# Kernel optimization log

Measured on AMD Instinct MI355X. Metric: run time of the kernel, lower is better.

## Reference

```python
import jax, jax.numpy as jnp
import numpy as np
from jax import lax

B, HCH, NCODES, H, W = 16, 32, 256, 256, 256

def conv2d(x, w, b, pad):
    y = lax.conv_general_dilated(x, w, (1, 1), [(pad, pad), (pad, pad)],
                                 dimension_numbers=('NCHW', 'OIHW', 'NCHW'))
    return y + b[None, :, None, None]

def vq(z, codebook):
    # z: (B,C,H,W); codebook: (K,C)
    zf = jnp.transpose(z, (0, 2, 3, 1)).reshape(-1, z.shape[1])  # (BHW,C)
    dists = (zf ** 2).sum(1, keepdims=True) + (codebook ** 2).sum(1) - 2.0 * zf @ codebook.T
    idx = jnp.argmin(dists, axis=1)
    zq = codebook[idx].reshape(z.shape[0], z.shape[2], z.shape[3], z.shape[1])
    zq = jnp.transpose(zq, (0, 3, 1, 2))
    # straight-through estimator
    return z + lax.stop_gradient(zq - z)

def setup_inputs() -> dict:
    key = jax.random.key(0)
    ks = jax.random.split(key, 12)
    s = lambda k, shp, scale=0.1: (jax.random.normal(k, shp, jnp.float32) * scale)
    return {
        'x': jax.random.normal(ks[0], (B, 1, H, W), jnp.float32),
        'stem_w': s(ks[1], (HCH, 1, 3, 3)),
        'stem_b': s(ks[2], (HCH,)),
        'up1_w': s(ks[3], (HCH, HCH, 3, 3)),
        'up1_b': s(ks[4], (HCH,)),
        'up2_w': s(ks[5], (HCH, HCH, 1, 1)),
        'up2_b': s(ks[6], (HCH,)),
        'tau_w': s(ks[7], (HCH, HCH, 1, 1)),
        'tau_b': s(ks[8], (HCH,)),
        'codebook': jax.random.uniform(ks[9], (NCODES, HCH), jnp.float32,
                                       -1.0 / NCODES, 1.0 / NCODES),
        'dec_w': s(ks[10], (1, HCH, 1, 1)),
        'dec_b': s(ks[11], (1,)),
        'n_steps': 5,
    }

def reference(x, stem_w, stem_b, up1_w, up1_b, up2_w, up2_b, tau_w, tau_b,
              codebook, dec_w, dec_b, n_steps):
    state = jax.nn.relu(conv2d(x, stem_w, stem_b, 1))
    for t in range(n_steps):
        delta = conv2d(jax.nn.relu(conv2d(state, up1_w, up1_b, 1)), up2_w, up2_b, 0)
        beta = jax.nn.sigmoid(conv2d(state, tau_w, tau_b, 0))
        state = beta * state + (1.0 - beta) * delta
        state = vq(state, codebook)  # vq_every = 1
    return jax.nn.sigmoid(conv2d(state, dec_w, dec_b, 0))
```

## Files before the change

kernel.cpp:

```cpp
#include <hip/hip_runtime.h>
#include <hip/hip_bf16.h>

#define BATCH 16
#define HH 256
#define WW 256
#define NPIX (BATCH*HH*WW)
#define NSTEPS 5
#define CBS 40
#define HS  258
#define HIMG (HS*HS)

#define W1P 0
#define W2P 9216
#define WTP 10240
#define IDP 11264
#define CBP 12288
#define FRAGS_TOT 20480

using u16 = unsigned short;
using u32 = unsigned int;
using u8  = unsigned char;

typedef __attribute__((ext_vector_type(8))) short bf8_t;
typedef __attribute__((ext_vector_type(4))) float f4_t;
typedef __attribute__((ext_vector_type(2))) float f2_t;

#define MFMA16 __builtin_amdgcn_mfma_f32_16x16x32_bf16

#define DPPMIN(v, CTRL) do { \
    u32 _o = (u32)__builtin_amdgcn_update_dpp((int)(v), (int)(v), (CTRL), 0xF, 0xF, false); \
    (v) = _o < (v) ? _o : (v); } while (0)

#define LDS_ORDER() asm volatile("" ::: "memory")

__device__ __forceinline__ float bf2f(u32 u) {
    union { u32 i; float f; } v; v.i = u << 16; return v.f;
}
__device__ __forceinline__ u16 f2bf(float f) {
    union { float f; u32 i; } v; v.f = f;
    u32 x = v.i;
    x += 0x7fffu + ((x >> 16) & 1u);
    return (u16)(x >> 16);
}
__device__ __forceinline__ u32 pack2bf(float a, float b) {
    __hip_bfloat162 h2 = __float22bfloat162_rn(float2{a, b});
    union { __hip_bfloat162 h; u32 u; } v; v.h = h2; return v.u;
}
__device__ __forceinline__ float ldin(const void* p, int i, int f32) {
    return f32 ? ((const float*)p)[i] : bf2f(((const u16*)p)[i]);
}
__device__ __forceinline__ u16 ldbf(const void* p, int i, int f32) {
    return f32 ? f2bf(((const float*)p)[i]) : ((const u16*)p)[i];
}
__device__ __forceinline__ int sniff_f32(const void* xraw) {
    const u32* xw = (const u32*)xraw;
    int cnt = 0;
    for (int j = 0; j < 64; j++) {
        u32 w = xw[j];
        float flo = bf2f(w & 0xffffu);
        float a = fabsf(flo);
        if (flo == 0.0f || (a >= 6e-8f && a <= 64.0f)) cnt++;
    }
    return (cnt < 32) ? 1 : 0;
}
__device__ __forceinline__ int chperm(int kp) { return (kp >> 1) | ((kp & 1) << 4); }

__global__ void prep_kernel(const void* x,
    const void* stem_w, const void* stem_b, const void* up1_w, const void* up1_b,
    const void* up2_w, const void* up2_b, const void* tau_w, const void* tau_b,
    const void* cb, const void* dec_w, const void* dec_b,
    u16* frags, u16* cb_bf, u16* idxh_a, u16* idxh_b,
    float* cn2, float* cadj, float* decdot, float* wf0,
    float* up1_bf, float* up2_bf, float* tau_bf, float* stem_bf, int* flag)
{
    int f32 = sniff_f32(x);
    int i = blockIdx.x * 256 + threadIdx.x;
    if (i == 0) *flag = f32;
    if (i < 9216) {
        int slot = i >> 9, rem = i & 511, lane = rem >> 3, j = rem & 7;
        int tap = slot >> 1, nt = slot & 1;
        int co = nt*16 + (lane & 15), ci = chperm((lane >> 4)*8 + j);
        frags[W1P + i] = ldbf(up1_w, (co*32+ci)*9 + tap, f32);
        return;
    }
    i -= 9216;
    if (i < 1024) {
        int nt = i >> 9, rem = i & 511, lane = rem >> 3, j = rem & 7;
        int co = nt*16 + (lane & 15), k = chperm((lane >> 4)*8 + j);
        frags[W2P + i] = f2bf(-0.25f * ldin(up2_w, co*32 + k, f32));
        return;
    }
    i -= 1024;
    if (i < 1024) {
        int nt = i >> 9, rem = i & 511, lane = rem >> 3, j = rem & 7;
        int co = nt*16 + (lane & 15), k = chperm((lane >> 4)*8 + j);
        frags[WTP + i] = ldbf(tau_w, co*32 + k, f32);
        return;
    }
    i -= 1024;
    if (i < 1024) {
        int s = i >> 9, rem = i & 511, lane = rem >> 3, j = rem & 7;
        int colq = lane & 15, quad = lane >> 4;
        int ch = chperm(quad*8 + j);
        frags[IDP + i] = (ch == (colq + s*16)) ? (u16)0xBE80 : (u16)0;
        return;
    }
    i -= 1024;
    if (i < 8192) {
        int nt = i >> 9, rem = i & 511, lane = rem >> 3, j = rem & 7;
        int code = nt*16 + (lane & 15), c = chperm((lane >> 4)*8 + j);
        frags[CBP + i] = ldbf(cb, code*32 + c, f32);
        return;
    }
    i -= 8192;
    if (i < 257*CBS) {
        int row = i / CBS, p = i - row*CBS;
        cb_bf[i] = (p < 32 && row < 256) ? ldbf(cb, row*32 + chperm(p), f32) : (u16)0;
        return;
    }
    i -= 257*CBS;
    if (i < 16448) {
        int bb = i / 1028, r = i - bb*1028;
        int row, colh;
        if (r < 258)      { row = 0;            colh = r; }
        else if (r < 516) { row = 257;          colh = r - 258; }
        else if (r < 774) { row = r - 516 + 1;  colh = 0; }
        else              { row = r - 774 + 1;  colh = 257; }
        int a = bb*HIMG + row*HS + colh;
        idxh_a[a] = 256; idxh_b[a] = 256;
        return;
    }
    i -= 16448;
    if (i < 256) {
        float s = 0.f;
        for (int c = 0; c < 32; c++) { float v = ldin(cb, i*32+c, f32); s += v*v; }
        cn2[i] = 0.5f * s;
        return;
    }
    i -= 256;
    if (i < 256) {
        float s = 0.f;
        for (int c = 0; c < 32; c++) { float v = ldin(cb, i*32+c, f32); s += v*v; }
        cadj[i] = 0.25f * (0.5f * s) + 0.5f;
        return;
    }
    i -= 256;
    if (i < 256) {
        float s = ldin(dec_b, 0, f32);
        for (int c = 0; c < 32; c++) s += ldin(dec_w, c, f32) * ldin(cb, i*32+c, f32);
        decdot[i] = s;
        return;
    }
    i -= 256;
    if (i < 288) {
        int tap = i >> 5, e = i & 31;
        int co = (e >> 1) + (e & 1)*16;
        wf0[i] = ldin(stem_w, co*9 + tap, f32);
        return;
    }
    i -= 288;
    if (i < 32) { up1_bf[i]  = ldin(up1_b, i, f32); return; }
    i -= 32;
    if (i < 32) { up2_bf[i]  = -0.25f * ldin(up2_b, i, f32); return; }
    i -= 32;
    if (i < 32) { tau_bf[i]  = ldin(tau_b, i, f32); return; }
    i -= 32;
    if (i < 32) {
        int co = (i >> 1) + (i & 1)*16;
        stem_bf[i] = ldin(stem_b, co, f32);
        return;
    }
}

__global__ __launch_bounds__(512) void step0_kernel(
    const void* __restrict__ xraw, const int* __restrict__ flagp,
    u16* __restrict__ idx_out,
    const u16* __restrict__ fragsg, const float* __restrict__ cn2,
    const float* __restrict__ up1_b, const float* __restrict__ up2_b,
    const float* __restrict__ tau_b, const float* __restrict__ wf0,
    const float* __restrict__ stem_bf)
{
    __shared__ __align__(16) u16 smem[34944];
    u16* w1f   = smem;
    u16* w2f   = smem + 9216;
    u16* wtf   = smem + 10240;
    u16* tileq = smem + 11264;
    u16* hzb   = smem + 30848;
    float* xs  = (float*)hzb;

    const u16* __restrict__ cbg = fragsg + CBP;

    int tid = threadIdx.x;
    int lane = tid & 63, wave = tid >> 6;
    int col = lane & 15, quad = lane >> 4;
    int b = blockIdx.z, x0 = blockIdx.x * 16, y0 = blockIdx.y * 32;

    bf8_t id0 = *(const bf8_t*)&fragsg[IDP + (0*64+lane)*8];
    bf8_t id1 = *(const bf8_t*)&fragsg[IDP + (1*64+lane)*8];

    {
        const uint4* s4 = (const uint4*)(fragsg + W1P);
        uint4* d4 = (uint4*)smem;
        for (int i = tid; i < 1408; i += 512) d4[i] = s4[i];
    }

    {
        int f32 = *flagp;
        for (int pp = tid; pp < 720; pp += 512) {
            int r = pp / 20, c = pp - r*20;
            int gy = y0 - 2 + r, gx = x0 - 2 + c;
            float v = 0.f;
            if ((unsigned)gy < 256u && (unsigned)gx < 256u)
                v = ldin(xraw, (b << 16) | (gy << 8) | gx, f32);
            xs[pp] = v;
        }
        __syncthreads();
        const f2_t* wb2 = (const f2_t*)stem_bf;
        for (int pp = tid; pp < 612; pp += 512) {
            int r = pp / 18, c = pp - r*18;
            int gy = y0 - 1 + r, gx = x0 - 1 + c;
            uint4 qv[4] = {{0,0,0,0},{0,0,0,0},{0,0,0,0},{0,0,0,0}};
            if ((unsigned)gy < 256u && (unsigned)gx < 256u) {
                f2_t acc2[16];
#pragma unroll
                for (int m = 0; m < 16; m++) acc2[m] = wb2[m];
#pragma unroll
                for (int tap = 0; tap < 9; tap++) {
                    float v = xs[(r + tap/3)*20 + (c + tap%3)];
                    f2_t vv = {v, v};
                    const f2_t* w2 = (const f2_t*)&wf0[tap*32];
#pragma unroll
                    for (int m = 0; m < 16; m++)
                        acc2[m] = __builtin_elementwise_fma(vv, w2[m], acc2[m]);
                }
                u32* ow = (u32*)qv;
#pragma unroll
                for (int m = 0; m < 16; m++)
                    ow[m] = pack2bf(fmaxf(acc2[m][0], 0.f), fmaxf(acc2[m][1], 0.f));
            }
#pragma unroll
            for (int q = 0; q < 4; q++)
                *(uint4*)&tileq[(q*612 + pp)*8] = qv[q];
        }
    }
    __syncthreads();

    float cn2adj[16];
#pragma unroll
    for (int nt = 0; nt < 16; nt++) cn2adj[nt] = 0.25f*cn2[nt*16+col] + 0.5f;
    float bu1C0 = up1_b[col], bu1C1 = up1_b[col+16];
    float bu2_0 = up2_b[col], bu2_1 = up2_b[col+16];
    float bt0 = tau_b[col],   bt1 = tau_b[col+16];
    u16* hzw = &hzb[wave*512];
    u32* hz32 = (u32*)hzw;
    int wy = wave * 4;
    f4_t kz = {0.f,0.f,0.f,0.f};

    bf8_t rows[4][3];
#pragma unroll
    for (int i = 0; i < 4; i++)
#pragma unroll
        for (int dx = 0; dx < 3; dx++)
            rows[i][dx] = *(const bf8_t*)&tileq[(quad*612 + (wy+i)*18 + col+dx)*8];

#pragma unroll
    for (int rrp = 0; rrp < 2; rrp++) {
        if (rrp) {
#pragma unroll
            for (int dx = 0; dx < 3; dx++) {
                rows[0][dx] = rows[2][dx];
                rows[1][dx] = rows[3][dx];
                rows[2][dx] = *(const bf8_t*)&tileq[(quad*612 + (wy+4)*18 + col+dx)*8];
                rows[3][dx] = *(const bf8_t*)&tileq[(quad*612 + (wy+5)*18 + col+dx)*8];
            }
        }
        f4_t aA0 = kz, aA1 = kz, aB0 = kz, aB1 = kz;
#pragma unroll
        for (int t = 0; t < 9; t++) {
            int dy = t/3, dx = t - dy*3;
            bf8_t wA = *(const bf8_t*)&w1f[((t*2+0)*64 + lane)*8];
            bf8_t wB = *(const bf8_t*)&w1f[((t*2+1)*64 + lane)*8];
            aA0 = MFMA16(rows[dy  ][dx], wA, aA0, 0, 0, 0);
            aA1 = MFMA16(rows[dy  ][dx], wB, aA1, 0, 0, 0);
            aB0 = MFMA16(rows[dy+1][dx], wA, aB0, 0, 0, 0);
            aB1 = MFMA16(rows[dy+1][dx], wB, aB1, 0, 0, 0);
        }
#pragma unroll
        for (int r = 0; r < 4; r++) {
            int px = quad*4 + r;
            hz32[px*16 + col] = pack2bf(fmaxf(aA0[r] + bu1C0, 0.f),
                                        fmaxf(aA1[r] + bu1C1, 0.f));
        }
        LDS_ORDER();
        bf8_t hA0 = *(const bf8_t*)&hzw[col*32 + quad*8];
        LDS_ORDER();
#pragma unroll
        for (int r = 0; r < 4; r++) {
            int px = quad*4 + r;
            hz32[px*16 + col] = pack2bf(fmaxf(aB0[r] + bu1C0, 0.f),
                                        fmaxf(aB1[r] + bu1C1, 0.f));
        }
        LDS_ORDER();
        bf8_t hA1 = *(const bf8_t*)&hzw[col*32 + quad*8];
        LDS_ORDER();

        bf8_t w20 = *(const bf8_t*)&w2f[(0*64+lane)*8];
        bf8_t w21 = *(const bf8_t*)&w2f[(1*64+lane)*8];
        bf8_t wt0 = *(const bf8_t*)&wtf[(0*64+lane)*8];
        bf8_t wt1 = *(const bf8_t*)&wtf[(1*64+lane)*8];
        bf8_t sA0 = rows[1][1], sA1 = rows[2][1];
        f4_t d00 = MFMA16(hA0, w20, kz, 0, 0, 0);
        f4_t d01 = MFMA16(hA0, w21, kz, 0, 0, 0);
        f4_t d10 = MFMA16(hA1, w20, kz, 0, 0, 0);
        f4_t d11 = MFMA16(hA1, w21, kz, 0, 0, 0);
        f4_t t00 = MFMA16(sA0, wt0, kz, 0, 0, 0);
        f4_t t01 = MFMA16(sA0, wt1, kz, 0, 0, 0);
        f4_t t10 = MFMA16(sA1, wt0, kz, 0, 0, 0);
        f4_t t11 = MFMA16(sA1, wt1, kz, 0, 0, 0);
        f4_t S0l = MFMA16(sA0, id0, kz, 0, 0, 0);
        f4_t S0h = MFMA16(sA0, id1, kz, 0, 0, 0);
        f4_t S1l = MFMA16(sA1, id0, kz, 0, 0, 0);
        f4_t S1h = MFMA16(sA1, id1, kz, 0, 0, 0);

#pragma unroll
        for (int r = 0; r < 4; r++) {
            int px = quad*4 + r;
            float dl0 = d00[r] + bu2_0, tv0 = t00[r] + bt0;
            float be0 = 1.0f / (1.0f + __expf(-tv0));
            float dl1 = d01[r] + bu2_1, tv1 = t01[r] + bt1;
            float be1 = 1.0f / (1.0f + __expf(-tv1));
            hz32[px*16 + col] = pack2bf(dl0 + be0*(S0l[r] - dl0),
                                        dl1 + be1*(S0h[r] - dl1));
        }
        LDS_ORDER();
        bf8_t zA0 = *(const bf8_t*)&hzw[col*32 + quad*8];
        LDS_ORDER();
#pragma unroll
        for (int r = 0; r < 4; r++) {
            int px = quad*4 + r;
            float dl0 = d10[r] + bu2_0, tv0 = t10[r] + bt0;
            float be0 = 1.0f / (1.0f + __expf(-tv0));
            float dl1 = d11[r] + bu2_1, tv1 = t11[r] + bt1;
            float be1 = 1.0f / (1.0f + __expf(-tv1));
            hz32[px*16 + col] = pack2bf(dl0 + be0*(S1l[r] - dl0),
                                        dl1 + be1*(S1h[r] - dl1));
        }
        LDS_ORDER();
        bf8_t zA1 = *(const bf8_t*)&hzw[col*32 + quad*8];
        LDS_ORDER();

        u32 b0[4], b1[4];
#pragma unroll
        for (int r = 0; r < 4; r++) { b0[r] = 0xFFFFFFFFu; b1[r] = 0xFFFFFFFFu; }
#pragma unroll 4
        for (int nt = 0; nt < 16; nt++) {
            bf8_t cf = *(const bf8_t*)&cbg[(nt*64 + lane)*8];
            f4_t ci = {cn2adj[nt], cn2adj[nt], cn2adj[nt], cn2adj[nt]};
            f4_t s0 = MFMA16(zA0, cf, ci, 0, 0, 0);
            f4_t s1 = MFMA16(zA1, cf, ci, 0, 0, 0);
            u32 code = (u32)(nt*16) | (u32)col;
#pragma unroll
            for (int r = 0; r < 4; r++) {
                u32 k0 = (__builtin_bit_cast(u32, s0[r]) & 0xFFFFFF00u) | code;
                u32 k1 = (__builtin_bit_cast(u32, s1[r]) & 0xFFFFFF00u) | code;
                b0[r] = k0 < b0[r] ? k0 : b0[r];
                b1[r] = k1 < b1[r] ? k1 : b1[r];
            }
        }
#pragma unroll
        for (int r = 0; r < 4; r++) {
            DPPMIN(b0[r], 0x121); DPPMIN(b0[r], 0x122);
            DPPMIN(b0[r], 0x124); DPPMIN(b0[r], 0x128);
            DPPMIN(b1[r], 0x121); DPPMIN(b1[r], 0x122);
            DPPMIN(b1[r], 0x124); DPPMIN(b1[r], 0x128);
        }
        int yr = y0 + wy + rrp*2;
        if (col < 4) {
            int xc = x0 + quad*4 + col + 1;
            idx_out[b*HIMG + (yr+1)*HS + xc] = (u16)(b0[col] & 255u);
            idx_out[b*HIMG + (yr+2)*HS + xc] = (u16)(b1[col] & 255u);
        }
    }
}

__global__ __launch_bounds__(512) void step1_kernel(
    const u16* __restrict__ idx_in, u16* __restrict__ idx_out,
    const u16* __restrict__ fragsg, const u16* __restrict__ cbr_g,
    const float* __restrict__ cadj_g,
    const float* __restrict__ up1_b, const float* __restrict__ up2_b,
    const float* __restrict__ tau_b,
    const float* __restrict__ decdot, const int* __restrict__ flagp,
    void* __restrict__ out, int last)
{
    __shared__ __align__(16) u16 smem[26152];
    u16* w1f = smem;
    u16* w2f = smem + 9216;
    u16* wtf = smem + 10240;
    u16* cbr = smem + 11264;
    float* cadjf = (float*)(smem + 21544);
    u16* hzb = smem + 22056;

    int tid = threadIdx.x;
    int lane = tid & 63, wave = tid >> 6;
    int col = lane & 15, quad = lane >> 4;
    int b = blockIdx.z, x0 = blockIdx.x * 16, y0 = blockIdx.y * 32;
    int wy = wave * 4;

    bf8_t id0 = *(const bf8_t*)&fragsg[IDP + (0*64+lane)*8];
    bf8_t id1 = *(const bf8_t*)&fragsg[IDP + (1*64+lane)*8];

    u32 kp[6];
#pragma unroll
    for (int tr = 0; tr < 6; tr++) {
        int base = b*HIMG + (y0 + wy + tr)*HS + x0 + col;
        kp[tr] = (u32)idx_in[base]
               | ((u32)idx_in[base + 1] << 9)
               | ((u32)idx_in[base + 2] << 18);
    }

    {
        const uint4* s4 = (const uint4*)(fragsg + W1P);
        uint4* d4 = (uint4*)smem;
        for (int i = tid; i < 1408; i += 512) d4[i] = s4[i];
        const uint4* c4 = (const uint4*)cbr_g;
        uint4* e4 = (uint4*)cbr;
        for (int i = tid; i < 1285; i += 512) e4[i] = c4[i];
        const uint4* a4 = (const uint4*)cadj_g;
        uint4* f4p = (uint4*)cadjf;
        if (tid < 64) f4p[tid] = a4[tid];
    }
    __syncthreads();

    float bu1C0 = up1_b[col], bu1C1 = up1_b[col+16];
    float bu2_0 = up2_b[col], bu2_1 = up2_b[col+16];
    float bt0 = tau_b[col],   bt1 = tau_b[col+16];
    u16* hzw = &hzb[wave*512];
    u32* hz32 = (u32*)hzw;
    f4_t kz = {0.f,0.f,0.f,0.f};

    f4_t acc[4][2];
#pragma unroll
    for (int r4 = 0; r4 < 4; r4++) { acc[r4][0] = kz; acc[r4][1] = kz; }
    bf8_t sA[4];
#pragma unroll
    for (int dx = 0; dx < 3; dx++) {
        bf8_t F[6];
#pragma unroll
        for (int tr = 0; tr < 6; tr++) {
            int k = (int)((kp[tr] >> (9*dx)) & 511u);
            F[tr] = *(const bf8_t*)&cbr[k*CBS + quad*8];
        }
        if (dx == 1) {
#pragma unroll
            for (int r4 = 0; r4 < 4; r4++) sA[r4] = F[r4+1];
        }
#pragma unroll
        for (int dy = 0; dy < 3; dy++) {
            int t = dy*3 + dx;
            bf8_t wA = *(const bf8_t*)&w1f[((t*2+0)*64 + lane)*8];
            bf8_t wB = *(const bf8_t*)&w1f[((t*2+1)*64 + lane)*8];
#pragma unroll
            for (int r4 = 0; r4 < 4; r4++) {
                acc[r4][0] = MFMA16(F[r4+dy], wA, acc[r4][0], 0, 0, 0);
                acc[r4][1] = MFMA16(F[r4+dy], wB, acc[r4][1], 0, 0, 0);
            }
        }
    }

    bf8_t w20 = *(const bf8_t*)&w2f[(0*64+lane)*8];
    bf8_t w21 = *(const bf8_t*)&w2f[(1*64+lane)*8];
    bf8_t wt0 = *(const bf8_t*)&wtf[(0*64+lane)*8];
    bf8_t wt1 = *(const bf8_t*)&wtf[(1*64+lane)*8];

    bf8_t zA[4];
#pragma unroll
    for (int r4 = 0; r4 < 4; r4++) {
#pragma unroll
        for (int r = 0; r < 4; r++) {
            int px = quad*4 + r;
            hz32[px*16 + col] = pack2bf(fmaxf(acc[r4][0][r] + bu1C0, 0.f),
                                        fmaxf(acc[r4][1][r] + bu1C1, 0.f));
        }
        LDS_ORDER();
        bf8_t hA = *(const bf8_t*)&hzw[col*32 + quad*8];
        LDS_ORDER();
        f4_t d0 = MFMA16(hA, w20, kz, 0, 0, 0);
        f4_t d1 = MFMA16(hA, w21, kz, 0, 0, 0);
        f4_t t0 = MFMA16(sA[r4], wt0, kz, 0, 0, 0);
        f4_t t1 = MFMA16(sA[r4], wt1, kz, 0, 0, 0);
        f4_t Sl = MFMA16(sA[r4], id0, kz, 0, 0, 0);
        f4_t Sh = MFMA16(sA[r4], id1, kz, 0, 0, 0);
#pragma unroll
        for (int r = 0; r < 4; r++) {
            int px = quad*4 + r;
            float dl0 = d0[r] + bu2_0, tv0 = t0[r] + bt0;
            float be0 = 1.0f / (1.0f + __expf(-tv0));
            float dl1 = d1[r] + bu2_1, tv1 = t1[r] + bt1;
            float be1 = 1.0f / (1.0f + __expf(-tv1));
            hz32[px*16 + col] = pack2bf(dl0 + be0*(Sl[r] - dl0),
                                        dl1 + be1*(Sh[r] - dl1));
        }
        LDS_ORDER();
        zA[r4] = *(const bf8_t*)&hzw[col*32 + quad*8];
        LDS_ORDER();
    }

    u32 bk[4][4];
#pragma unroll
    for (int r4 = 0; r4 < 4; r4++)
#pragma unroll
        for (int r = 0; r < 4; r++) bk[r4][r] = 0xFFFFFFFFu;
#pragma unroll
    for (int nt = 0; nt < 16; nt++) {
        bf8_t cf = *(const bf8_t*)&cbr[(nt*16 + col)*CBS + quad*8];
        float ca = cadjf[nt*16 + col];
        f4_t ci = {ca, ca, ca, ca};
        u32 code = (u32)(nt*16) | (u32)col;
#pragma unroll
        for (int r4 = 0; r4 < 4; r4++) {
            f4_t sc = MFMA16(zA[r4], cf, ci, 0, 0, 0);
#pragma unroll
            for (int r = 0; r < 4; r++) {
                u32 k0 = (__builtin_bit_cast(u32, sc[r]) & 0xFFFFFF00u) | code;
                bk[r4][r] = k0 < bk[r4][r] ? k0 : bk[r4][r];
            }
        }
    }
    if (last) {
        int f32o = *flagp;
#pragma unroll
        for (int r4 = 0; r4 < 4; r4++) {
#pragma unroll
            for (int r = 0; r < 4; r++) {
                DPPMIN(bk[r4][r], 0x121); DPPMIN(bk[r4][r], 0x122);
                DPPMIN(bk[r4][r], 0x124); DPPMIN(bk[r4][r], 0x128);
            }
            int yr = y0 + wy + r4;
            if (col < 4) {
                float s = decdot[bk[r4][col] & 255u];
                float rv = 1.0f / (1.0f + __expf(-s));
                int p = ((b*256 + yr) << 8) + x0 + quad*4 + col;
                if (f32o) ((float*)out)[p] = rv;
                else      ((u16*)out)[p]   = f2bf(rv);
            }
        }
    } else {
#pragma unroll
        for (int r4 = 0; r4 < 4; r4++) {
#pragma unroll
            for (int r = 0; r < 4; r++) {
                DPPMIN(bk[r4][r], 0x121); DPPMIN(bk[r4][r], 0x122);
                DPPMIN(bk[r4][r], 0x124); DPPMIN(bk[r4][r], 0x128);
            }
            int yr = y0 + wy + r4;
            if (col < 4)
                idx_out[b*HIMG + (yr+1)*HS + (x0 + quad*4 + col + 1)] =
                    (u16)(bk[r4][col] & 255u);
        }
    }
}

extern "C" void kernel_launch(void* const* d_in, const int* in_sizes, int n_in,
                              void* d_out, int out_size, void* d_ws, size_t ws_size,
                              hipStream_t stream)
{
    const void* x      = d_in[0];
    const void* stem_w = d_in[1];
    const void* stem_b = d_in[2];
    const void* up1_w  = d_in[3];
    const void* up1_b  = d_in[4];
    const void* up2_w  = d_in[5];
    const void* up2_b  = d_in[6];
    const void* tau_w  = d_in[7];
    const void* tau_b  = d_in[8];
    const void* cb     = d_in[9];
    const void* dec_w  = d_in[10];
    const void* dec_b  = d_in[11];

    char* ws = (char*)d_ws;
    size_t off = 0;
    auto carve = [&](size_t bytes) -> void* {
        void* p = ws + off;
        off += (bytes + 255) & ~(size_t)255;
        return p;
    };
    u16*   idxA    = (u16*)  carve((size_t)BATCH*HIMG*2);
    u16*   idxB    = (u16*)  carve((size_t)BATCH*HIMG*2);
    u16*   frags   = (u16*)  carve(FRAGS_TOT * 2);
    u16*   cb_bf   = (u16*)  carve(257*CBS * 2);
    float* cn2     = (float*)carve(256 * 4);
    float* cadj    = (float*)carve(256 * 4);
    float* decdot  = (float*)carve(256 * 4);
    float* wf0     = (float*)carve(288 * 4);
    float* up1_bf  = (float*)carve(32 * 4);
    float* up2_bf  = (float*)carve(32 * 4);
    float* tau_bf  = (float*)carve(32 * 4);
    float* stem_bf = (float*)carve(32 * 4);
    int*   flag    = (int*)  carve(4);

    prep_kernel<<<190, 256, 0, stream>>>(x, stem_w, stem_b, up1_w, up1_b,
        up2_w, up2_b, tau_w, tau_b, cb, dec_w, dec_b,
        frags, cb_bf, idxA, idxB, cn2, cadj, decdot, wf0,
        up1_bf, up2_bf, tau_bf, stem_bf, flag);

    dim3 g0(WW/16, HH/32, BATCH);
    step0_kernel<<<g0, 512, 0, stream>>>(x, flag, idxA,
        frags, cn2, up1_bf, up2_bf, tau_bf, wf0, stem_bf);
    dim3 g1(WW/16, HH/32, BATCH);
    u16* cur = idxA; u16* nxt = idxB;
    for (int t = 1; t < NSTEPS; t++) {
        int last = (t == NSTEPS - 1) ? 1 : 0;
        step1_kernel<<<g1, 512, 0, stream>>>(cur, nxt, frags, cb_bf, cadj,
                                             up1_bf, up2_bf, tau_bf,
                                             decdot, flag, d_out, last);
        u16* tmp = cur; cur = nxt; nxt = tmp;
    }
}
```

Before: 375.1 us.

## Swap MFMA operand order to keep activations in registers and skip LDS transposes

Every MFMA now takes weights as the A operand and activations as B, so the output tile is channel-major. Its per-lane accumulator values can then be packed directly into the next MFMA's bf16 input fragment. This removes the per-wave LDS scratch buffer and the write-then-read transposes between the conv stages and before the codebook search. The argmin now reduces four codes per lane in registers plus a cross-quad swizzle/bpermute, replacing 16 DPP min chains. Step0 now reads the precomputed cadj array instead of cn2. Correctness relies on the bias vectors and cadj being laid out to match the new channel-major accumulator order.

Result: no change. 374.4 us (-0.2%).

```diff
diff --git a/kernel.cpp b/kernel.cpp
--- a/kernel.cpp
+++ b/kernel.cpp
@@ -27,12 +27,6 @@
 
 #define MFMA16 __builtin_amdgcn_mfma_f32_16x16x32_bf16
 
-#define DPPMIN(v, CTRL) do { \
-    u32 _o = (u32)__builtin_amdgcn_update_dpp((int)(v), (int)(v), (CTRL), 0xF, 0xF, false); \
-    (v) = _o < (v) ? _o : (v); } while (0)
-
-#define LDS_ORDER() asm volatile("" ::: "memory")
-
 __device__ __forceinline__ float bf2f(u32 u) {
     union { u32 i; float f; } v; v.i = u << 16; return v.f;
 }
@@ -64,6 +58,16 @@
     return (cnt < 32) ? 1 : 0;
 }
 __device__ __forceinline__ int chperm(int kp) { return (kp >> 1) | ((kp & 1) << 4); }
+
+__device__ __forceinline__ u32 xquad_min(u32 m, int lane) {
+    u32 o = (u32)__builtin_amdgcn_ds_swizzle((int)m, 0x401F);
+    m = o < m ? o : m;
+    u32 o2 = (u32)__builtin_amdgcn_ds_bpermute(((lane ^ 32) << 2), (int)m);
+    m = o2 < m ? o2 : m;
+    return m;
+}
+
+union UB { u32 w[4]; bf8_t v; };
 
 __global__ void prep_kernel(const void* x,
     const void* stem_w, const void* stem_b, const void* up1_w, const void* up1_b,
@@ -175,18 +179,17 @@
 __global__ __launch_bounds__(512) void step0_kernel(
     const void* __restrict__ xraw, const int* __restrict__ flagp,
     u16* __restrict__ idx_out,
-    const u16* __restrict__ fragsg, const float* __restrict__ cn2,
+    const u16* __restrict__ fragsg, const float* __restrict__ cadj,
     const float* __restrict__ up1_b, const float* __restrict__ up2_b,
     const float* __restrict__ tau_b, const float* __restrict__ wf0,
     const float* __restrict__ stem_bf)
 {
-    __shared__ __align__(16) u16 smem[34944];
+    __shared__ __align__(16) u16 smem[32288];
     u16* w1f   = smem;
     u16* w2f   = smem + 9216;
     u16* wtf   = smem + 10240;
     u16* tileq = smem + 11264;
-    u16* hzb   = smem + 30848;
-    float* xs  = (float*)hzb;
+    float* xs  = (float*)(smem + 30848);
 
     const u16* __restrict__ cbg = fragsg + CBP;
 
@@ -245,14 +248,12 @@
     }
     __syncthreads();
 
-    float cn2adj[16];
-#pragma unroll
-    for (int nt = 0; nt < 16; nt++) cn2adj[nt] = 0.25f*cn2[nt*16+col] + 0.5f;
-    float bu1C0 = up1_b[col], bu1C1 = up1_b[col+16];
-    float bu2_0 = up2_b[col], bu2_1 = up2_b[col+16];
-    float bt0 = tau_b[col],   bt1 = tau_b[col+16];
-    u16* hzw = &hzb[wave*512];
-    u32* hz32 = (u32*)hzw;
+    f4_t b1lo = *(const f4_t*)&up1_b[quad*4];
+    f4_t b1hi = *(const f4_t*)&up1_b[quad*4+16];
+    f4_t b2lo = *(const f4_t*)&up2_b[quad*4];
+    f4_t b2hi = *(const f4_t*)&up2_b[quad*4+16];
+    f4_t btlo = *(const f4_t*)&tau_b[quad*4];
+    f4_t bthi = *(const f4_t*)&tau_b[quad*4+16];
     int wy = wave * 4;
     f4_t kz = {0.f,0.f,0.f,0.f};
 
@@ -280,105 +281,78 @@
             int dy = t/3, dx = t - dy*3;
             bf8_t wA = *(const bf8_t*)&w1f[((t*2+0)*64 + lane)*8];
             bf8_t wB = *(const bf8_t*)&w1f[((t*2+1)*64 + lane)*8];
-            aA0 = MFMA16(rows[dy  ][dx], wA, aA0, 0, 0, 0);
-            aA1 = MFMA16(rows[dy  ][dx], wB, aA1, 0, 0, 0);
-            aB0 = MFMA16(rows[dy+1][dx], wA, aB0, 0, 0, 0);
-            aB1 = MFMA16(rows[dy+1][dx], wB, aB1, 0, 0, 0);
-        }
+            aA0 = MFMA16(wA, rows[dy  ][dx], aA0, 0, 0, 0);
+            aA1 = MFMA16(wB, rows[dy  ][dx], aA1, 0, 0, 0);
+            aB0 = MFMA16(wA, rows[dy+1][dx], aB0, 0, 0, 0);
+            aB1 = MFMA16(wB, rows[dy+1][dx], aB1, 0, 0, 0);
+        }
+        UB h0u, h1u;
 #pragma unroll
         for (int r = 0; r < 4; r++) {
-            int px = quad*4 + r;
-            hz32[px*16 + col] = pack2bf(fmaxf(aA0[r] + bu1C0, 0.f),
-                                        fmaxf(aA1[r] + bu1C1, 0.f));
-        }
-        LDS_ORDER();
-        bf8_t hA0 = *(const bf8_t*)&hzw[col*32 + quad*8];
-        LDS_ORDER();
-#pragma unroll
-        for (int r = 0; r < 4; r++) {
-            int px = quad*4 + r;
-            hz32[px*16 + col] = pack2bf(fmaxf(aB0[r] + bu1C0, 0.f),
-                                        fmaxf(aB1[r] + bu1C1, 0.f));
-        }
-        LDS_ORDER();
-        bf8_t hA1 = *(const bf8_t*)&hzw[col*32 + quad*8];
-        LDS_ORDER();
+            h0u.w[r] = pack2bf(fmaxf(aA0[r] + b1lo[r], 0.f),
+                               fmaxf(aA1[r] + b1hi[r], 0.f));
+            h1u.w[r] = pack2bf(fmaxf(aB0[r] + b1lo[r], 0.f),
+                               fmaxf(aB1[r] + b1hi[r], 0.f));
+        }
+        bf8_t hA0 = h0u.v, hA1 = h1u.v;
 
         bf8_t w20 = *(const bf8_t*)&w2f[(0*64+lane)*8];
         bf8_t w21 = *(const bf8_t*)&w2f[(1*64+lane)*8];
         bf8_t wt0 = *(const bf8_t*)&wtf[(0*64+lane)*8];
         bf8_t wt1 = *(const bf8_t*)&wtf[(1*64+lane)*8];
         bf8_t sA0 = rows[1][1], sA1 = rows[2][1];
-        f4_t d00 = MFMA16(hA0, w20, kz, 0, 0, 0);
-        f4_t d01 = MFMA16(hA0, w21, kz, 0, 0, 0);
-        f4_t d10 = MFMA16(hA1, w20, kz, 0, 0, 0);
-        f4_t d11 = MFMA16(hA1, w21, kz, 0, 0, 0);
-        f4_t t00 = MFMA16(sA0, wt0, kz, 0, 0, 0);
-        f4_t t01 = MFMA16(sA0, wt1, kz, 0, 0, 0);
-        f4_t t10 = MFMA16(sA1, wt0, kz, 0, 0, 0);
-        f4_t t11 = MFMA16(sA1, wt1, kz, 0, 0, 0);
-        f4_t S0l = MFMA16(sA0, id0, kz, 0, 0, 0);
-        f4_t S0h = MFMA16(sA0, id1, kz, 0, 0, 0);
-        f4_t S1l = MFMA16(sA1, id0, kz, 0, 0, 0);
-        f4_t S1h = MFMA16(sA1, id1, kz, 0, 0, 0);
-
+        f4_t d00 = MFMA16(w20, hA0, kz, 0, 0, 0);
+        f4_t d01 = MFMA16(w21, hA0, kz, 0, 0, 0);
+        f4_t d10 = MFMA16(w20, hA1, kz, 0, 0, 0);
+        f4_t d11 = MFMA16(w21, hA1, kz, 0, 0, 0);
+        f4_t t00 = MFMA16(wt0, sA0, kz, 0, 0, 0);
+        f4_t t01 = MFMA16(wt1, sA0, kz, 0, 0, 0);
+        f4_t t10 = MFMA16(wt0, sA1, kz, 0, 0, 0);
+        f4_t t11 = MFMA16(wt1, sA1, kz, 0, 0, 0);
+        f4_t S0l = MFMA16(id0, sA0, kz, 0, 0, 0);
+        f4_t S0h = MFMA16(id1, sA0, kz, 0, 0, 0);
+        f4_t S1l = MFMA16(id0, sA1, kz, 0, 0, 0);
+        f4_t S1h = MFMA16(id1, sA1, kz, 0, 0, 0);
+
+        UB z0u, z1u;
 #pragma unroll
         for (int r = 0; r < 4; r++) {
-            int px = quad*4 + r;
-            float dl0 = d00[r] + bu2_0, tv0 = t00[r] + bt0;
+            float dl0 = d00[r] + b2lo[r], tv0 = t00[r] + btlo[r];
             float be0 = 1.0f / (1.0f + __expf(-tv0));
-            float dl1 = d01[r] + bu2_1, tv1 = t01[r] + bt1;
+            float dl1 = d01[r] + b2hi[r], tv1 = t01[r] + bthi[r];
             float be1 = 1.0f / (1.0f + __expf(-tv1));
-            hz32[px*16 + col] = pack2bf(dl0 + be0*(S0l[r] - dl0),
-                                        dl1 + be1*(S0h[r] - dl1));
-        }
-        LDS_ORDER();
-        bf8_t zA0 = *(const bf8_t*)&hzw[col*32 + quad*8];
-        LDS_ORDER();
-#pragma unroll
-        for (int r = 0; r < 4; r++) {
-            int px = quad*4 + r;
-            float dl0 = d10[r] + bu2_0, tv0 = t10[r] + bt0;
-            float be0 = 1.0f / (1.0f + __expf(-tv0));
-            float dl1 = d11[r] + bu2_1, tv1 = t11[r] + bt1;
-            float be1 = 1.0f / (1.0f + __expf(-tv1));
-            hz32[px*16 + col] = pack2bf(dl0 + be0*(S1l[r] - dl0),
-                                        dl1 + be1*(S1h[r] - dl1));
-        }
-        LDS_ORDER();
-        bf8_t zA1 = *(const bf8_t*)&hzw[col*32 + quad*8];
-        LDS_ORDER();
-
-        u32 b0[4], b1[4];
-#pragma unroll
-        for (int r = 0; r < 4; r++) { b0[r] = 0xFFFFFFFFu; b1[r] = 0xFFFFFFFFu; }
+            z0u.w[r] = pack2bf(dl0 + be0*(S0l[r] - dl0), dl1 + be1*(S0h[r] - dl1));
+            float el0 = d10[r] + b2lo[r], sv0 = t10[r] + btlo[r];
+            float ce0 = 1.0f / (1.0f + __expf(-sv0));
+            float el1 = d11[r] + b2hi[r], sv1 = t11[r] + bthi[r];
+            float ce1 = 1.0f / (1.0f + __expf(-sv1));
+            z1u.w[r] = pack2bf(el0 + ce0*(S1l[r] - el0), el1 + ce1*(S1h[r] - el1));
+        }
+        bf8_t zA0 = z0u.v, zA1 = z1u.v;
+
+        u32 b0 = 0xFFFFFFFFu, b1 = 0xFFFFFFFFu;
 #pragma unroll 4
         for (int nt = 0; nt < 16; nt++) {
             bf8_t cf = *(const bf8_t*)&cbg[(nt*64 + lane)*8];
-            f4_t ci = {cn2adj[nt], cn2adj[nt], cn2adj[nt], cn2adj[nt]};
-            f4_t s0 = MFMA16(zA0, cf, ci, 0, 0, 0);
-            f4_t s1 = MFMA16(zA1, cf, ci, 0, 0, 0);
-            u32 code = (u32)(nt*16) | (u32)col;
+            f4_t ci = *(const f4_t*)&cadj[nt*16 + quad*4];
+            f4_t s0 = MFMA16(cf, zA0, ci, 0, 0, 0);
+            f4_t s1 = MFMA16(cf, zA1, ci, 0, 0, 0);
+            u32 codebase = (u32)(nt*16 + quad*4);
 #pragma unroll
             for (int r = 0; r < 4; r++) {
-                u32 k0 = (__builtin_bit_cast(u32, s0[r]) & 0xFFFFFF00u) | code;
-                u32 k1 = (__builtin_bit_cast(u32, s1[r]) & 0xFFFFFF00u) | code;
-                b0[r] = k0 < b0[r] ? k0 : b0[r];
-                b1[r] = k1 < b1[r] ? k1 : b1[r];
+                u32 k0 = (__builtin_bit_cast(u32, s0[r]) & 0xFFFFFF00u) | (codebase + r);
+                u32 k1 = (__builtin_bit_cast(u32, s1[r]) & 0xFFFFFF00u) | (codebase + r);
+                b0 = k0 < b0 ? k0 : b0;
+                b1 = k1 < b1 ? k1 : b1;
             }
         }
-#pragma unroll
-        for (int r = 0; r < 4; r++) {
-            DPPMIN(b0[r], 0x121); DPPMIN(b0[r], 0x122);
-            DPPMIN(b0[r], 0x124); DPPMIN(b0[r], 0x128);
-            DPPMIN(b1[r], 0x121); DPPMIN(b1[r], 0x122);
-            DPPMIN(b1[r], 0x124); DPPMIN(b1[r], 0x128);
-        }
+        b0 = xquad_min(b0, lane);
+        b1 = xquad_min(b1, lane);
         int yr = y0 + wy + rrp*2;
-        if (col < 4) {
-            int xc = x0 + quad*4 + col + 1;
-            idx_out[b*HIMG + (yr+1)*HS + xc] = (u16)(b0[col] & 255u);
-            idx_out[b*HIMG + (yr+2)*HS + xc] = (u16)(b1[col] & 255u);
+        if (quad == 0) {
+            int xc = x0 + col + 1;
+            idx_out[b*HIMG + (yr+1)*HS + xc] = (u16)(b0 & 255u);
+            idx_out[b*HIMG + (yr+2)*HS + xc] = (u16)(b1 & 255u);
         }
     }
 }
@@ -392,13 +366,12 @@
     const float* __restrict__ decdot, const int* __restrict__ flagp,
     void* __restrict__ out, int last)
 {
-    __shared__ __align__(16) u16 smem[26152];
+    __shared__ __align__(16) u16 smem[22056];
     u16* w1f = smem;
     u16* w2f = smem + 9216;
     u16* wtf = smem + 10240;
     u16* cbr = smem + 11264;
     float* cadjf = (float*)(smem + 21544);
-    u16* hzb = smem + 22056;
 
     int tid = threadIdx.x;
     int lane = tid & 63, wave = tid >> 6;
@@ -431,11 +404,12 @@
     }
     __syncthreads();
 
-    float bu1C0 = up1_b[col], bu1C1 = up1_b[col+16];
-    float bu2_0 = up2_b[col], bu2_1 = up2_b[col+16];
-    float bt0 = tau_b[col],   bt1 = tau_b[col+16];
-    u16* hzw = &hzb[wave*512];
-    u32* hz32 = (u32*)hzw;
+    f4_t b1lo = *(const f4_t*)&up1_b[quad*4];
+    f4_t b1hi = *(const f4_t*)&up1_b[quad*4+16];
+    f4_t b2lo = *(const f4_t*)&up2_b[quad*4];
+    f4_t b2hi = *(const f4_t*)&up2_b[quad*4+16];
+    f4_t btlo = *(const f4_t*)&tau_b[quad*4];
+    f4_t bthi = *(const f4_t*)&tau_b[quad*4+16];
     f4_t kz = {0.f,0.f,0.f,0.f};
 
     f4_t acc[4][2];
@@ -461,8 +435,8 @@
             bf8_t wB = *(const bf8_t*)&w1f[((t*2+1)*64 + lane)*8];
 #pragma unroll
             for (int r4 = 0; r4 < 4; r4++) {
-                acc[r4][0] = MFMA16(F[r4+dy], wA, acc[r4][0], 0, 0, 0);
-                acc[r4][1] = MFMA16(F[r4+dy], wB, acc[r4][1], 0, 0, 0);
+                acc[r4][0] = MFMA16(wA, F[r4+dy], acc[r4][0], 0, 0, 0);
+                acc[r4][1] = MFMA16(wB, F[r4+dy], acc[r4][1], 0, 0, 0);
             }
         }
     }
@@ -475,71 +449,60 @@
     bf8_t zA[4];
 #pragma unroll
     for (int r4 = 0; r4 < 4; r4++) {
+        UB hu;
+#pragma unroll
+        for (int r = 0; r < 4; r++)
+            hu.w[r] = pack2bf(fmaxf(acc[r4][0][r] + b1lo[r], 0.f),
+                              fmaxf(acc[r4][1][r] + b1hi[r], 0.f));
+        bf8_t hA = hu.v;
+        f4_t d0 = MFMA16(w20, hA, kz, 0, 0, 0);
+        f4_t d1 = MFMA16(w21, hA, kz, 0, 0, 0);
+        f4_t t0 = MFMA16(wt0, sA[r4], kz, 0, 0, 0);
+        f4_t t1 = MFMA16(wt1, sA[r4], kz, 0, 0, 0);
+        f4_t Sl = MFMA16(id0, sA[r4], kz, 0, 0, 0);
+        f4_t Sh = MFMA16(id1, sA[r4], kz, 0, 0, 0);
+        UB zu;
 #pragma unroll
         for (int r = 0; r < 4; r++) {
-            int px = quad*4 + r;
-            hz32[px*16 + col] = pack2bf(fmaxf(acc[r4][0][r] + bu1C0, 0.f),
-                                        fmaxf(acc[r4][1][r] + bu1C1, 0.f));
-        }
-        LDS_ORDER();
-        bf8_t hA = *(const bf8_t*)&hzw[col*32 + quad*8];
-        LDS_ORDER();
-        f4_t d0 = MFMA16(hA, w20, kz, 0, 0, 0);
-        f4_t d1 = MFMA16(hA, w21, kz, 0, 0, 0);
-        f4_t t0 = MFMA16(sA[r4], wt0, kz, 0, 0, 0);
-        f4_t t1 = MFMA16(sA[r4], wt1, kz, 0, 0, 0);
-        f4_t Sl = MFMA16(sA[r4], id0, kz, 0, 0, 0);
-        f4_t Sh = MFMA16(sA[r4], id1, kz, 0, 0, 0);
-#pragma unroll
-        for (int r = 0; r < 4; r++) {
-            int px = quad*4 + r;
-            float dl0 = d0[r] + bu2_0, tv0 = t0[r] + bt0;
+            float dl0 = d0[r] + b2lo[r], tv0 = t0[r] + btlo[r];
             float be0 = 1.0f / (1.0f + __expf(-tv0));
-            float dl1 = d1[r] + bu2_1, tv1 = t1[r] + bt1;
+            float dl1 = d1[r] + b2hi[r], tv1 = t1[r] + bthi[r];
             float be1 = 1.0f / (1.0f + __expf(-tv1));
-            hz32[px*16 + col] = pack2bf(dl0 + be0*(Sl[r] - dl0),
-                                        dl1 + be1*(Sh[r] - dl1));
-        }
-        LDS_ORDER();
-        zA[r4] = *(const bf8_t*)&hzw[col*32 + quad*8];
-        LDS_ORDER();
-    }
-
-    u32 bk[4][4];
-#pragma unroll
-    for (int r4 = 0; r4 < 4; r4++)
-#pragma unroll
-        for (int r = 0; r < 4; r++) bk[r4][r] = 0xFFFFFFFFu;
+            zu.w[r] = pack2bf(dl0 + be0*(Sl[r] - dl0), dl1 + be1*(Sh[r] - dl1));
+        }
+        zA[r4] = zu.v;
+    }
+
+    u32 bk[4];
+#pragma unroll
+    for (int r4 = 0; r4 < 4; r4++) bk[r4] = 0xFFFFFFFFu;
 #pragma unroll
     for (int nt = 0; nt < 16; nt++) {
         bf8_t cf = *(const bf8_t*)&cbr[(nt*16 + col)*CBS + quad*8];
-        float ca = cadjf[nt*16 + col];
-        f4_t ci = {ca, ca, ca, ca};
-        u32 code = (u32)(nt*16) | (u32)col;
+        f4_t ci = *(const f4_t*)&cadjf[nt*16 + quad*4];
+        u32 codebase = (u32)(nt*16 + quad*4);
 #pragma unroll
         for (int r4 = 0; r4 < 4; r4++) {
-            f4_t sc = MFMA16(zA[r4], cf, ci, 0, 0, 0);
+            f4_t sc = MFMA16(cf, zA[r4], ci, 0, 0, 0);
 #pragma unroll
             for (int r = 0; r < 4; r++) {
-                u32 k0 = (__builtin_bit_cast(u32, sc[r]) & 0xFFFFFF00u) | code;
-                bk[r4][r] = k0 < bk[r4][r] ? k0 : bk[r4][r];
+                u32 k0 = (__builtin_bit_cast(u32, sc[r]) & 0xFFFFFF00u) | (codebase + r);
+                bk[r4] = k0 < bk[r4] ? k0 : bk[r4];
             }
         }
     }
+#pragma unroll
+    for (int r4 = 0; r4 < 4; r4++) bk[r4] = xquad_min(bk[r4], lane);
+
     if (last) {
         int f32o = *flagp;
 #pragma unroll
         for (int r4 = 0; r4 < 4; r4++) {
-#pragma unroll
-            for (int r = 0; r < 4; r++) {
-                DPPMIN(bk[r4][r], 0x121); DPPMIN(bk[r4][r], 0x122);
-                DPPMIN(bk[r4][r], 0x124); DPPMIN(bk[r4][r], 0x128);
-            }
             int yr = y0 + wy + r4;
-            if (col < 4) {
-                float s = decdot[bk[r4][col] & 255u];
+            if (quad == 0) {
+                float s = decdot[bk[r4] & 255u];
                 float rv = 1.0f / (1.0f + __expf(-s));
-                int p = ((b*256 + yr) << 8) + x0 + quad*4 + col;
+                int p = ((b*256 + yr) << 8) + x0 + col;
                 if (f32o) ((float*)out)[p] = rv;
                 else      ((u16*)out)[p]   = f2bf(rv);
             }
@@ -547,15 +510,9 @@
     } else {
 #pragma unroll
         for (int r4 = 0; r4 < 4; r4++) {
-#pragma unroll
-            for (int r = 0; r < 4; r++) {
-                DPPMIN(bk[r4][r], 0x121); DPPMIN(bk[r4][r], 0x122);
-                DPPMIN(bk[r4][r], 0x124); DPPMIN(bk[r4][r], 0x128);
-            }
             int yr = y0 + wy + r4;
-            if (col < 4)
-                idx_out[b*HIMG + (yr+1)*HS + (x0 + quad*4 + col + 1)] =
-                    (u16)(bk[r4][col] & 255u);
+            if (quad == 0)
+                idx_out[b*HIMG + (yr+1)*HS + (x0 + col + 1)] = (u16)(bk[r4] & 255u);
         }
     }
 }
@@ -605,7 +562,7 @@
 
     dim3 g0(WW/16, HH/32, BATCH);
     step0_kernel<<<g0, 512, 0, stream>>>(x, flag, idxA,
-        frags, cn2, up1_bf, up2_bf, tau_bf, wf0, stem_bf);
+        frags, cadj, up1_bf, up2_bf, tau_bf, wf0, stem_bf);
     dim3 g1(WW/16, HH/32, BATCH);
     u16* cur = idxA; u16* nxt = idxB;
     for (int t = 1; t < NSTEPS; t++) {
```
